# Performance work log

Hardware: AMD Instinct MI355X
Metric: run time of the kernel (lower is better)

## Reference

```python
import jax, jax.numpy as jnp
import numpy as np

SCORER_BIAS = 0.0
LN_EPS = 1e-5


def setup_inputs() -> dict:
    key = jax.random.key(0)
    k0, k1, k2 = jax.random.split(key, 3)
    B, L, D, H = 8, 8192, 1024, 256
    features = jax.random.normal(k0, (B, L, D), dtype=jnp.float32)
    gamma = jnp.ones((D,), jnp.float32)
    beta = jnp.zeros((D,), jnp.float32)
    W1 = (jax.random.normal(k1, (D, H)) * (1.0 / np.sqrt(D))).astype(jnp.float32)
    b1 = jnp.zeros((H,), jnp.float32)
    W2 = (jax.random.normal(k2, (H, 1)) * (1.0 / np.sqrt(H))).astype(jnp.float32)
    b2 = jnp.zeros((1,), jnp.float32)
    return {"features": features, "gamma": gamma, "beta": beta,
            "W1": W1, "b1": b1, "W2": W2, "b2": b2, "k": 512}


def reference(features, gamma, beta, W1, b1, W2, b2, k):
    # LayerNorm over last dim D
    mu = jnp.mean(features, axis=-1, keepdims=True)
    var = jnp.mean(jnp.square(features - mu), axis=-1, keepdims=True)
    x = (features - mu) * jax.lax.rsqrt(var + LN_EPS) * gamma + beta  # [B,L,D]
    # small MLP scorer: Linear -> GELU(exact, matches torch default) -> Linear
    h = jax.nn.gelu(jnp.einsum('bld,dh->blh', x, W1) + b1, approximate=False)
    scores = (jnp.einsum('blh,ho->blo', h, W2) + b2)[..., 0] + SCORER_BIAS  # [B,L]
    # per-row top-k (torch.topk semantics: largest, sorted)
    _, idx = jax.lax.top_k(scores, k)  # [B,k] int32
    # batched gather of original (un-normalized) features
    selected = jnp.take_along_axis(features, idx[..., None], axis=1)  # [B,k,D]
    return selected, scores, idx
```

## Files before the change

### kernel.cpp

```cpp
#include <hip/hip_runtime.h>
#include <math.h>

#define Dk 1024
#define Hk 256
#define Lk 8192
#define Bk 8
#define MTOT (Bk*Lk)

typedef _Float16 f16;
typedef __attribute__((ext_vector_type(8))) _Float16 f16x8;
typedef __attribute__((ext_vector_type(4))) _Float16 f16x4;
typedef __attribute__((ext_vector_type(16))) float f32x16;
typedef unsigned long long u64;

#define BSTEP 16384
#define AR 20
#define APL (128*AR)
#define ABUF (4*APL)

#define GLD_LDS16(g, l)                                                        \
  __builtin_amdgcn_global_load_lds(                                            \
      (const __attribute__((address_space(1))) unsigned int*)(g),              \
      (__attribute__((address_space(3))) unsigned int*)(l), 16, 0, 0)

__global__ __launch_bounds__(1024) void prep_split(
    const float* __restrict__ W1, const float* __restrict__ gamma,
    const float* __restrict__ beta, f16* __restrict__ W1F,
    float* __restrict__ Spart, float* __restrict__ Tpart) {
  __shared__ float ps[1024], pt[1024];
  const int b = blockIdx.x, t = threadIdx.x;
  float sa = 0.f, ta = 0.f;
  #pragma unroll
  for (int j = 0; j < 4; ++j) {
    int idx = j * 65536 + b * 1024 + t;
    int d = idx >> 8, h = idx & 255;
    float w = W1[idx];
    float g = gamma[d];
    sa = fmaf(g, w, sa);
    ta = fmaf(beta[d], w, ta);
    float wg = g * w;
    f16 whi = (f16)wg;
    f16 wlp = (f16)((wg - (float)whi) * 2048.f);
    int s = d >> 5, kc = (d >> 4) & 1, kh = (d >> 3) & 1, kk = d & 7;
    int cb = h >> 5, c = h & 31;
    size_t base = (size_t)s * BSTEP + ((size_t)kc * 8 + cb) * 512
                + (kh * 32 + c) * 8 + kk;
    W1F[base] = whi;
    W1F[base + 8192] = wlp;
  }
  ps[t] = sa; pt[t] = ta;
  __syncthreads();
  if (t < 256) {
    Spart[b * 256 + t] = ps[t] + ps[t + 256] + ps[t + 512] + ps[t + 768];
    Tpart[b * 256 + t] = pt[t] + pt[t + 256] + pt[t + 512] + pt[t + 768];
  }
}

__global__ __launch_bounds__(256) void prep_combine(
    const float* __restrict__ Spart, const float* __restrict__ Tpart,
    const float* __restrict__ b1, float* __restrict__ S, float* __restrict__ Tb) {
  int j = threadIdx.x;
  float s = 0.f, t = 0.f;
  for (int b = 0; b < 64; ++b) { s += Spart[b * 256 + j]; t += Tpart[b * 256 + j]; }
  S[j] = s;
  Tb[j] = t + b1[j];
}

#define MM3(aA, aB, ah, ax, wh, wl)                                            \
  aA = __builtin_amdgcn_mfma_f32_32x32x16_f16(ah, wh, aA, 0, 0, 0);            \
  aB = __builtin_amdgcn_mfma_f32_32x32x16_f16(ah, wl, aB, 0, 0, 0);            \
  aB = __builtin_amdgcn_mfma_f32_32x32x16_f16(ax, wh, aB, 0, 0, 0);

__global__ __launch_bounds__(1024) void scores_mfma(
    const float* __restrict__ F, const f16* __restrict__ W1F,
    const float* __restrict__ S, const float* __restrict__ Tb,
    const float* __restrict__ W2, const float* __restrict__ b2,
    float* __restrict__ scores_out) {
  __shared__ __align__(16) f16 As[2][ABUF];
  __shared__ __align__(16) f16 Bs[3][BSTEP];
  __shared__ float smu[128], srs[128];
  __shared__ float sred[128][4];

  const int tid = threadIdx.x;
  const int RM = blockIdx.x * 128;
  const int w = tid >> 6, lane = tid & 63;
  const int rg = w & 3;
  const int cg = w >> 2;
  const int c31 = lane & 31, kh = lane >> 5;

  const int arow = tid >> 3, kq = tid & 7;
  const int akc = kq >> 2, akoff = (kq & 3) * 4;
  const int aw0 = (akc * 128 + arow) * AR + akoff;
  const float* Aptr = F + (size_t)(RM + arow) * Dk + kq * 4;

  const int ar0 = (rg * 32 + c31) * AR + kh * 8;
  const int br0 = (cg * 2) * 512 + lane * 8;

  f32x16 accA[2], accB[2];
  accA[0] = (f32x16)(0.f); accB[0] = (f32x16)(0.f);
  accA[1] = (f32x16)(0.f); accB[1] = (f32x16)(0.f);

  float rsum = 0.f, rsq = 0.f;

#define SPLIT4(buf, fv)                                                        \
  {                                                                            \
    f16x4 vhi, vlo;                                                            \
    _Pragma("unroll")                                                          \
    for (int e = 0; e < 4; ++e) {                                              \
      float x = (e == 0) ? fv.x : (e == 1) ? fv.y : (e == 2) ? fv.z : fv.w;    \
      rsum += x; rsq = fmaf(x, x, rsq);                                        \
      f16 hi = (f16)x;                                                         \
      vhi[e] = hi;                                                             \
      vlo[e] = (f16)((x - (float)hi) * 2048.f);                                \
    }                                                                          \
    *reinterpret_cast<f16x4*>(&As[buf][aw0])           = vhi;                  \
    *reinterpret_cast<f16x4*>(&As[buf][aw0 + 2 * APL]) = vlo;                  \
  }

#define STEP_BARRIER()                                                         \
  asm volatile("s_waitcnt vmcnt(3) lgkmcnt(0)" ::: "memory");                  \
  __builtin_amdgcn_s_barrier();                                                \
  asm volatile("" ::: "memory");

  GLD_LDS16(W1F + (size_t)tid * 8, &Bs[0][tid * 8]);
  GLD_LDS16(W1F + (size_t)(1024 + tid) * 8, &Bs[0][8192 + tid * 8]);
  GLD_LDS16(W1F + BSTEP + (size_t)tid * 8, &Bs[1][tid * 8]);
  GLD_LDS16(W1F + BSTEP + (size_t)(1024 + tid) * 8, &Bs[1][8192 + tid * 8]);
  float4 av = *reinterpret_cast<const float4*>(Aptr);
  SPLIT4(0, av)
  av = *reinterpret_cast<const float4*>(Aptr + 32);
  asm volatile("s_waitcnt vmcnt(3) lgkmcnt(0)" ::: "memory");
  __builtin_amdgcn_s_barrier();
  asm volatile("" ::: "memory");

  for (int s = 0; s < 32; ++s) {
    const int cur = s & 1;
    const int bcur = s % 3, bnxt = (s + 2) % 3;
    {
      const f16* bsrc = W1F + (size_t)((s + 2) < 32 ? (s + 2) : 0) * BSTEP;
      GLD_LDS16(bsrc + (size_t)tid * 8, &Bs[bnxt][tid * 8]);
      GLD_LDS16(bsrc + (size_t)(1024 + tid) * 8, &Bs[bnxt][8192 + tid * 8]);
    }
    if (s < 31) SPLIT4(cur ^ 1, av)
    av = *reinterpret_cast<const float4*>(s < 30 ? Aptr + (s + 2) * 32 : Aptr);
    #pragma unroll
    for (int kc = 0; kc < 2; ++kc) {
      const f16* ab = &As[cur][kc * APL + ar0];
      f16x4 h0 = *reinterpret_cast<const f16x4*>(ab);
      f16x4 h1 = *reinterpret_cast<const f16x4*>(ab + 4);
      f16x4 x0 = *reinterpret_cast<const f16x4*>(ab + 2 * APL);
      f16x4 x1 = *reinterpret_cast<const f16x4*>(ab + 2 * APL + 4);
      f16x8 ahi = __builtin_shufflevector(h0, h1, 0, 1, 2, 3, 4, 5, 6, 7);
      f16x8 axl = __builtin_shufflevector(x0, x1, 0, 1, 2, 3, 4, 5, 6, 7);
      #pragma unroll
      for (int nf = 0; nf < 2; ++nf) {
        const f16* bb = &Bs[bcur][kc * 4096 + nf * 512 + br0];
        f16x8 wh = *reinterpret_cast<const f16x8*>(bb);
        f16x8 wl = *reinterpret_cast<const f16x8*>(bb + 8192);
        MM3(accA[nf], accB[nf], ahi, axl, wh, wl)
      }
    }
    STEP_BARRIER()
  }

  __syncthreads();

  rsum += __shfl_xor(rsum, 1); rsum += __shfl_xor(rsum, 2); rsum += __shfl_xor(rsum, 4);
  rsq  += __shfl_xor(rsq, 1);  rsq  += __shfl_xor(rsq, 2);  rsq  += __shfl_xor(rsq, 4);
  if ((tid & 7) == 0) {
    float mu  = rsum * (1.f / 1024.f);
    float var = rsq * (1.f / 1024.f) - mu * mu;
    smu[arow] = mu;
    srs[arow] = rsqrtf(var + 1e-5f);
  }
  __syncthreads();

  float s2[2], tb2[2], w2v[2];
  #pragma unroll
  for (int nf = 0; nf < 2; ++nf) {
    int col = cg * 64 + nf * 32 + c31;
    s2[nf] = S[col]; tb2[nf] = Tb[col]; w2v[nf] = W2[col];
  }
  #pragma unroll
  for (int reg = 0; reg < 16; ++reg) {
    const int row = rg * 32 + (reg & 3) + 8 * (reg >> 2) + 4 * kh;
    float mu = smu[row], rs = srs[row];
    float part = 0.f;
    #pragma unroll
    for (int nf = 0; nf < 2; ++nf) {
      float val = accA[nf][reg] + accB[nf][reg] * (1.f / 2048.f);
      float hpre = rs * val - rs * mu * s2[nf] + tb2[nf];
      float g = 0.5f * hpre * (1.f + erff(hpre * 0.70710678118654752f));
      part = fmaf(g, w2v[nf], part);
    }
    part += __shfl_xor(part, 1); part += __shfl_xor(part, 2);
    part += __shfl_xor(part, 4); part += __shfl_xor(part, 8);
    part += __shfl_xor(part, 16);
    if (c31 == 0) sred[row][cg] = part;
  }
  __syncthreads();
  if (tid < 128) {
    float sc = b2[0] + sred[tid][0] + sred[tid][1] + sred[tid][2] + sred[tid][3];
    scores_out[RM + tid] = sc;
  }
}

__global__ __launch_bounds__(512) void topk_stage1(
    const float* __restrict__ scores, u64* __restrict__ kout) {
  __shared__ u64 keys[1024];
  const int blk = blockIdx.x;
  const int batch = blk >> 3, chunk = blk & 7;
  const int t = threadIdx.x;
  #pragma unroll
  for (int j = 0; j < 2; ++j) {
    int i = t + j * 512;
    int gi = chunk * 1024 + i;
    unsigned u = __float_as_uint(scores[(size_t)batch * Lk + gi]);
    unsigned mono = (u & 0x80000000u) ? ~u : (u | 0x80000000u);
    keys[i] = ((u64)(~mono) << 32) | (unsigned)gi;
  }
  __syncthreads();
  for (int size = 2; size <= 1024; size <<= 1) {
    for (int stride = size >> 1; stride > 0; stride >>= 1) {
      int lo = ((t & ~(stride - 1)) << 1) | (t & (stride - 1));
      int hi = lo + stride;
      bool up = ((lo & size) == 0);
      u64 a = keys[lo], c = keys[hi];
      if ((a > c) == up) { keys[lo] = c; keys[hi] = a; }
      __syncthreads();
    }
  }
  kout[(size_t)blk * 512 + t] = keys[t];
}

__global__ __launch_bounds__(512) void topk_stage2(
    const u64* __restrict__ kin, int k,
    float* __restrict__ idx_f, int* __restrict__ idx_i) {
  __shared__ u64 kk[4096];
  __shared__ u64 tmp[2048];
  const int b = blockIdx.x, t = threadIdx.x;
  #pragma unroll
  for (int j = 0; j < 8; ++j) kk[t + j * 512] = kin[(size_t)b * 4096 + t + j * 512];
  __syncthreads();
  #pragma unroll
  for (int j = 0; j < 4; ++j) {
    u64 a = kk[j * 1024 + t];
    u64 c = kk[j * 1024 + 512 + (511 - t)];
    tmp[j * 512 + t] = a < c ? a : c;
  }
  __syncthreads();
  for (int stride = 256; stride > 0; stride >>= 1) {
    #pragma unroll
    for (int w = 0; w < 2; ++w) {
      int p = t + w * 512;
      int r = p >> 8, q = p & 255;
      int lo = r * 512 + (((q & ~(stride - 1)) << 1) | (q & (stride - 1)));
      u64 a = tmp[lo], c = tmp[lo + stride];
      if (a > c) { tmp[lo] = c; tmp[lo + stride] = a; }
    }
    __syncthreads();
  }
  #pragma unroll
  for (int j = 0; j < 2; ++j) {
    u64 a = tmp[j * 1024 + t];
    u64 c = tmp[j * 1024 + 512 + (511 - t)];
    kk[j * 512 + t] = a < c ? a : c;
  }
  __syncthreads();
  for (int stride = 256; stride > 0; stride >>= 1) {
    int r = t >> 8, q = t & 255;
    int lo = r * 512 + (((q & ~(stride - 1)) << 1) | (q & (stride - 1)));
    u64 a = kk[lo], c = kk[lo + stride];
    if (a > c) { kk[lo] = c; kk[lo + stride] = a; }
    __syncthreads();
  }
  {
    u64 a = kk[t];
    u64 c = kk[512 + (511 - t)];
    tmp[t] = a < c ? a : c;
  }
  __syncthreads();
  for (int stride = 256; stride > 0; stride >>= 1) {
    if (t < 256) {
      int lo = ((t & ~(stride - 1)) << 1) | (t & (stride - 1));
      u64 a = tmp[lo], c = tmp[lo + stride];
      if (a > c) { tmp[lo] = c; tmp[lo + stride] = a; }
    }
    __syncthreads();
  }
  if (t < k) {
    int id = (int)(tmp[t] & 0xFFFFFFFFu);
    idx_f[(size_t)b * k + t] = (float)id;
    idx_i[(size_t)b * k + t] = id;
  }
}

__global__ __launch_bounds__(256) void gather_kernel(
    const float* __restrict__ F, const int* __restrict__ idx,
    float* __restrict__ out, int k) {
  int row = blockIdx.x;
  int b = row / k;
  int id = idx[row];
  const float4* src = reinterpret_cast<const float4*>(F + ((size_t)b * Lk + id) * Dk);
  float4* dst = reinterpret_cast<float4*>(out + (size_t)row * Dk);
  dst[threadIdx.x] = src[threadIdx.x];
}

extern "C" void kernel_launch(void* const* d_in, const int* in_sizes, int n_in,
                              void* d_out, int out_size, void* d_ws, size_t ws_size,
                              hipStream_t stream) {
  const float* F     = (const float*)d_in[0];
  const float* gamma = (const float*)d_in[1];
  const float* beta  = (const float*)d_in[2];
  const float* W1    = (const float*)d_in[3];
  const float* b1    = (const float*)d_in[4];
  const float* W2    = (const float*)d_in[5];
  const float* b2    = (const float*)d_in[6];
  int k = (out_size - Bk * Lk) / (Bk * Dk + Bk);

  float* out_sel = (float*)d_out;
  float* out_sc  = out_sel + (size_t)Bk * k * Dk;
  float* out_idx = out_sc + (size_t)Bk * Lk;

  f16*   W1F   = (f16*)d_ws;
  u64*   kout  = (u64*)((char*)d_ws + (1 << 20));
  float* Spart = (float*)((char*)kout + 262144);
  float* Tpart = Spart + 16384;
  float* Sp    = Tpart + 16384;
  float* Tbp   = Sp + Hk;
  int*   idxi  = (int*)(Tbp + Hk);

  hipLaunchKernelGGL(prep_split,   dim3(64),         dim3(1024), 0, stream,
                     W1, gamma, beta, W1F, Spart, Tpart);
  hipLaunchKernelGGL(prep_combine, dim3(1),          dim3(Hk),   0, stream,
                     Spart, Tpart, b1, Sp, Tbp);
  hipLaunchKernelGGL(scores_mfma,  dim3(MTOT / 128), dim3(1024), 0, stream,
                     F, W1F, Sp, Tbp, W2, b2, out_sc);
  hipLaunchKernelGGL(topk_stage1,  dim3(64),         dim3(512),  0, stream,
                     out_sc, kout);
  hipLaunchKernelGGL(topk_stage2,  dim3(Bk),         dim3(512),  0, stream,
                     kout, k, out_idx, idxi);
  hipLaunchKernelGGL(gather_kernel, dim3(Bk * k),    dim3(256),  0, stream,
                     F, idxi, out_sel, k);
}
```

Baseline: 169.1 us.

## Split each K-step into two ping-pong phases with setprio around MFMA clusters

Each 32-wide K step of the fused LayerNorm/W1 GEMM is split into two half-steps. In each half, the LDS fragment reads and one global-to-LDS weight load are issued first, then a barrier, then the MFMA cluster runs at raised wave priority (s_setprio) behind a sched_barrier. This aims to interleave memory issue and matrix math across waves, HipKittens-style, instead of doing all loads then all math. It adds extra barriers per step and relies on the waitcnt bookkeeping staying correct, with vmcnt(3) now checked only at the end of the step.

Measured after the change: 164.2 us. -2.9%, faster.

```diff
diff --git a/kernel.cpp b/kernel.cpp
--- a/kernel.cpp
+++ b/kernel.cpp
@@ -117,11 +117,6 @@
     *reinterpret_cast<f16x4*>(&As[buf][aw0 + 2 * APL]) = vlo;                  \
   }
 
-#define STEP_BARRIER()                                                         \
-  asm volatile("s_waitcnt vmcnt(3) lgkmcnt(0)" ::: "memory");                  \
-  __builtin_amdgcn_s_barrier();                                                \
-  asm volatile("" ::: "memory");
-
   GLD_LDS16(W1F + (size_t)tid * 8, &Bs[0][tid * 8]);
   GLD_LDS16(W1F + (size_t)(1024 + tid) * 8, &Bs[0][8192 + tid * 8]);
   GLD_LDS16(W1F + BSTEP + (size_t)tid * 8, &Bs[1][tid * 8]);
@@ -136,31 +131,58 @@
   for (int s = 0; s < 32; ++s) {
     const int cur = s & 1;
     const int bcur = s % 3, bnxt = (s + 2) % 3;
+    const f16* bsrc = W1F + (size_t)((s + 2) < 32 ? (s + 2) : 0) * BSTEP;
+
     {
-      const f16* bsrc = W1F + (size_t)((s + 2) < 32 ? (s + 2) : 0) * BSTEP;
-      GLD_LDS16(bsrc + (size_t)tid * 8, &Bs[bnxt][tid * 8]);
-      GLD_LDS16(bsrc + (size_t)(1024 + tid) * 8, &Bs[bnxt][8192 + tid * 8]);
-    }
-    if (s < 31) SPLIT4(cur ^ 1, av)
-    av = *reinterpret_cast<const float4*>(s < 30 ? Aptr + (s + 2) * 32 : Aptr);
-    #pragma unroll
-    for (int kc = 0; kc < 2; ++kc) {
-      const f16* ab = &As[cur][kc * APL + ar0];
+      const f16* ab = &As[cur][ar0];
       f16x4 h0 = *reinterpret_cast<const f16x4*>(ab);
       f16x4 h1 = *reinterpret_cast<const f16x4*>(ab + 4);
       f16x4 x0 = *reinterpret_cast<const f16x4*>(ab + 2 * APL);
       f16x4 x1 = *reinterpret_cast<const f16x4*>(ab + 2 * APL + 4);
       f16x8 ahi = __builtin_shufflevector(h0, h1, 0, 1, 2, 3, 4, 5, 6, 7);
       f16x8 axl = __builtin_shufflevector(x0, x1, 0, 1, 2, 3, 4, 5, 6, 7);
-      #pragma unroll
-      for (int nf = 0; nf < 2; ++nf) {
-        const f16* bb = &Bs[bcur][kc * 4096 + nf * 512 + br0];
-        f16x8 wh = *reinterpret_cast<const f16x8*>(bb);
-        f16x8 wl = *reinterpret_cast<const f16x8*>(bb + 8192);
-        MM3(accA[nf], accB[nf], ahi, axl, wh, wl)
-      }
-    }
-    STEP_BARRIER()
+      const f16* bb0 = &Bs[bcur][br0];
+      f16x8 wh0 = *reinterpret_cast<const f16x8*>(bb0);
+      f16x8 wl0 = *reinterpret_cast<const f16x8*>(bb0 + 8192);
+      f16x8 wh1 = *reinterpret_cast<const f16x8*>(bb0 + 512);
+      f16x8 wl1 = *reinterpret_cast<const f16x8*>(bb0 + 512 + 8192);
+      GLD_LDS16(bsrc + (size_t)tid * 8, &Bs[bnxt][tid * 8]);
+      if (s < 31) SPLIT4(cur ^ 1, av)
+      __builtin_amdgcn_s_barrier();
+      asm volatile("s_waitcnt lgkmcnt(0)" ::: "memory");
+      __builtin_amdgcn_sched_barrier(0);
+      __builtin_amdgcn_s_setprio(1);
+      MM3(accA[0], accB[0], ahi, axl, wh0, wl0)
+      MM3(accA[1], accB[1], ahi, axl, wh1, wl1)
+      __builtin_amdgcn_s_setprio(0);
+      __builtin_amdgcn_s_barrier();
+    }
+    {
+      const f16* ab = &As[cur][APL + ar0];
+      f16x4 h0 = *reinterpret_cast<const f16x4*>(ab);
+      f16x4 h1 = *reinterpret_cast<const f16x4*>(ab + 4);
+      f16x4 x0 = *reinterpret_cast<const f16x4*>(ab + 2 * APL);
+      f16x4 x1 = *reinterpret_cast<const f16x4*>(ab + 2 * APL + 4);
+      f16x8 ahi = __builtin_shufflevector(h0, h1, 0, 1, 2, 3, 4, 5, 6, 7);
+      f16x8 axl = __builtin_shufflevector(x0, x1, 0, 1, 2, 3, 4, 5, 6, 7);
+      const f16* bb1 = &Bs[bcur][4096 + br0];
+      f16x8 wh0 = *reinterpret_cast<const f16x8*>(bb1);
+      f16x8 wl0 = *reinterpret_cast<const f16x8*>(bb1 + 8192);
+      f16x8 wh1 = *reinterpret_cast<const f16x8*>(bb1 + 512);
+      f16x8 wl1 = *reinterpret_cast<const f16x8*>(bb1 + 512 + 8192);
+      GLD_LDS16(bsrc + (size_t)(1024 + tid) * 8, &Bs[bnxt][8192 + tid * 8]);
+      av = *reinterpret_cast<const float4*>(s < 30 ? Aptr + (s + 2) * 32 : Aptr);
+      __builtin_amdgcn_s_barrier();
+      asm volatile("s_waitcnt lgkmcnt(0)" ::: "memory");
+      __builtin_amdgcn_sched_barrier(0);
+      __builtin_amdgcn_s_setprio(1);
+      MM3(accA[0], accB[0], ahi, axl, wh0, wl0)
+      MM3(accA[1], accB[1], ahi, axl, wh1, wl1)
+      __builtin_amdgcn_s_setprio(0);
+      asm volatile("s_waitcnt vmcnt(3)" ::: "memory");
+      __builtin_amdgcn_s_barrier();
+      asm volatile("" ::: "memory");
+    }
   }
 
   __syncthreads();
```
